# Performance work log

Measured on AMD Instinct MI355X. Metric: run time of the kernel, lower is better.

## Reference

```python
import jax, jax.numpy as jnp
import numpy as np

B = 64           # batch size
N = 512          # number of nodes
E = 1            # edge feature dims of the GSO
M = 256          # nodes carrying edge-variant weights (hybrid EV since M < N)
F = [1, 8, 8]    # node-signal features per layer
K = [3, 3]       # shift taps per layer
MLP = [512, 128] # readout dims
P_EDGE = 0.03    # graph density
ZTOL = 1e-9      # zero tolerance for sparsity pattern


def setup_inputs():
    ks = jax.random.split(jax.random.key(0), 13)
    x = jax.random.normal(ks[0], (B, F[0], N), dtype=jnp.float32)
    adj = (jax.random.uniform(ks[1], (E, N, N)) < P_EDGE).astype(jnp.float32)
    S = adj * jax.random.normal(ks[2], (E, N, N), dtype=jnp.float32) / np.sqrt(N * P_EDGE)

    def w(k, shape, scale):
        return jax.random.normal(k, shape, dtype=jnp.float32) * np.float32(scale)

    wEV1 = w(ks[3], (F[1], E, K[0], F[0], N, N), 1.0 / np.sqrt(F[0] * N))
    wLSI1 = w(ks[4], (F[1], E, K[0], F[0]), 1.0 / np.sqrt(F[0] * K[0]))
    b1 = w(ks[5], (F[1], 1), 0.1)
    wEV2 = w(ks[6], (F[2], E, K[1], F[1], N, N), 1.0 / np.sqrt(F[1] * N))
    wLSI2 = w(ks[7], (F[2], E, K[1], F[1]), 1.0 / np.sqrt(F[1] * K[1]))
    b2 = w(ks[8], (F[2], 1), 0.1)
    W1 = w(ks[9], (MLP[0], F[2] * N), 1.0 / np.sqrt(F[2] * N))
    bW1 = w(ks[10], (MLP[0],), 0.1)
    W2 = w(ks[11], (MLP[1], MLP[0]), 1.0 / np.sqrt(MLP[0]))
    bW2 = w(ks[12], (MLP[1],), 0.1)
    return dict(x=x, S=S, wEV1=wEV1, wLSI1=wLSI1, b1=b1,
                wEV2=wEV2, wLSI2=wLSI2, b2=b2, W1=W1, bW1=bW1, W2=W2, bW2=bW2)


def _sparsity_mask(S):
    # support of S + I, then kill the [M:, M:] block (hybrid EV mask)
    eye = jnp.eye(N, dtype=S.dtype)
    sp = ((jnp.abs(S) + eye[None]) > ZTOL).astype(S.dtype)      # (E,N,N)
    hyb = jnp.ones((N, N), S.dtype).at[M:, M:].set(0.0)
    return sp * hyb[None]


def _ev_layer(xl, S, sp, wEV, wLSI, b):
    # xl: (B,G,N); wEV: (F,E,K,G,N,N); wLSI: (F,E,K,G); b: (F,1)
    Phi = wEV * sp[None, :, None, None]                          # masked filter matrices
    Kl = wEV.shape[2]
    # EV part: y = sum_k Phi^(k) ... Phi^(0) x, summed over e, g
    z = jnp.einsum('fegmn,bgn->bfegm', Phi[:, :, 0], xl)
    y = z
    for k in range(1, Kl):
        z = jnp.einsum('fegmn,bfegn->bfegm', Phi[:, :, k], z)
        y = y + z
    y = y.sum(axis=(2, 3))                                       # (B,F,N)
    # LSI part of the hybrid filter: sum_{e,k,g} h_{fekg} S_e^k x_g
    xe = jnp.broadcast_to(xl[:, None], (xl.shape[0], S.shape[0]) + xl.shape[1:])
    zs = [xe]                                                    # k = 0: identity
    for k in range(1, Kl):
        zs.append(jnp.einsum('emn,begn->begm', S, zs[-1]))
    zst = jnp.stack(zs, axis=2)                                  # (B,E,K,G,N)
    y = y + jnp.einsum('fekg,bekgn->bfn', wLSI, zst)
    return y + b[None]                                           # bias broadcast over nodes


def reference(x, S, wEV1, wLSI1, b1, wEV2, wLSI2, b2, W1, bW1, W2, bW2):
    sp = _sparsity_mask(S)
    # order=None -> permIdentity, so x[:, :, order] == x; NoPool is identity
    y = _ev_layer(x, S, sp, wEV1, wLSI1, b1)
    y = _ev_layer(y, S, sp, wEV2, wLSI2, b2)
    yf = y.reshape(y.shape[0], -1)                               # (B, F[-1]*N)
    h = yf @ W1.T + bW1                                          # linear MLP (no activation)
    return h @ W2.T + bW2
```

## Files before the change

### kernel.cpp

```cpp
#include <hip/hip_runtime.h>
#include <cstdint>
#include <cstddef>

#define NNODE 512
#define MMASK 256
#define ZT 1e-9f

__device__ __forceinline__ float rdl_f(float v, int l) {
  return __uint_as_float(__builtin_amdgcn_readlane(__float_as_uint(v), l));
}

__global__ __launch_bounds__(256) void k_prep(const float* __restrict__ x,
                                              const float* __restrict__ S,
                                              int* __restrict__ sp_col, int* __restrict__ sp_cnt,
                                              int* __restrict__ s_col, float* __restrict__ s_val,
                                              int* __restrict__ s_cnt,
                                              float* __restrict__ xt) {
  int gtid = blockIdx.x * 256 + threadIdx.x;
  int W = gtid >> 6, lane = threadIdx.x & 63;
  {
    int n = gtid >> 6, b = gtid & 63;
    xt[gtid] = x[b * NNODE + n];
  }
  int m = W;
  int csp = 0, cs = 0;
  unsigned long long lt = (1ull << lane) - 1ull;
  for (int ch = 0; ch < 8; ++ch) {
    int n = ch * 64 + lane;
    float s = S[m * NNODE + n];
    bool ps  = (s != 0.f);
    bool psp = ((fabsf(s) + ((m == n) ? 1.f : 0.f)) > ZT) && !((m >= MMASK) && (n >= MMASK));
    unsigned long long msp = __ballot(psp), ms = __ballot(ps);
    if (psp) { int p = csp + __popcll(msp & lt); if (p < 64) sp_col[(m << 6) + p] = n; }
    if (ps)  { int p = cs  + __popcll(ms  & lt); if (p < 64) { s_col[(m << 6) + p] = n; s_val[(m << 6) + p] = s; } }
    csp += __popcll(msp); cs += __popcll(ms);
  }
  if (lane >= csp) sp_col[(m << 6) + lane] = 0;
  if (lane >= cs)  { s_col[(m << 6) + lane] = 0; s_val[(m << 6) + lane] = 0.f; }
  if (lane == 0) { sp_cnt[m] = (csp < 64 ? csp : 64); s_cnt[m] = (cs < 64 ? cs : 64); }
}

__device__ __forceinline__ float ell_mac_rl(int clv, float wgv, int cnt,
                                            const float* __restrict__ zin, int lane) {
  float a0 = 0.f, a1 = 0.f, a2 = 0.f, a3 = 0.f;
  for (int base = 0; base < cnt; base += 16) {
#pragma unroll
    for (int i = 0; i < 16; i += 4) {
      int   c0 = __builtin_amdgcn_readlane(clv, base + i);
      int   c1 = __builtin_amdgcn_readlane(clv, base + i + 1);
      int   c2 = __builtin_amdgcn_readlane(clv, base + i + 2);
      int   c3 = __builtin_amdgcn_readlane(clv, base + i + 3);
      float w0 = rdl_f(wgv, base + i);
      float w1 = rdl_f(wgv, base + i + 1);
      float w2 = rdl_f(wgv, base + i + 2);
      float w3 = rdl_f(wgv, base + i + 3);
      a0 += w0 * zin[(c0 << 6) + lane];
      a1 += w1 * zin[(c1 << 6) + lane];
      a2 += w2 * zin[(c2 << 6) + lane];
      a3 += w3 * zin[(c3 << 6) + lane];
    }
  }
  return (a0 + a1) + (a2 + a3);
}

__device__ __forceinline__ float ell_mac_s(const int* __restrict__ cols,
                                           const float* __restrict__ ws,
                                           int cnt,
                                           const float* __restrict__ zin, int lane) {
  float a0 = 0.f, a1 = 0.f, a2 = 0.f, a3 = 0.f;
  for (int base = 0; base < cnt; base += 16) {
#pragma unroll
    for (int i = 0; i < 16; i += 4) {
      int   c0 = cols[base + i    ]; float w0 = ws[base + i    ];
      int   c1 = cols[base + i + 1]; float w1 = ws[base + i + 1];
      int   c2 = cols[base + i + 2]; float w2 = ws[base + i + 2];
      int   c3 = cols[base + i + 3]; float w3 = ws[base + i + 3];
      a0 += w0 * zin[(c0 << 6) + lane];
      a1 += w1 * zin[(c1 << 6) + lane];
      a2 += w2 * zin[(c2 << 6) + lane];
      a3 += w3 * zin[(c3 << 6) + lane];
    }
  }
  return (a0 + a1) + (a2 + a3);
}

__global__ __launch_bounds__(256) void k_l1s0(const float* __restrict__ wEV1,
    const int* __restrict__ sp_col, const int* __restrict__ sp_cnt,
    const int* __restrict__ s_col, const float* __restrict__ s_val, const int* __restrict__ s_cnt,
    const float* __restrict__ xt, float* __restrict__ zA1, float* __restrict__ u1) {
  int lane = threadIdx.x & 63;
  int W = __builtin_amdgcn_readfirstlane((blockIdx.x * 256 + (int)threadIdx.x) >> 6);
  int nwv = (gridDim.x << 2);
  for (int u = W; u < 4608; u += nwv) {
    if (u < 4096) {
      int f = u >> 9, r = u & 511;
      int clv = sp_col[(r << 6) + lane];
      int cnt = sp_cnt[r];
      const float* wrow = wEV1 + ((size_t)(f * 3 + 0) << 18) + ((size_t)r << 9);
      float wgv = (lane < cnt) ? wrow[clv] : 0.f;
      zA1[((size_t)f << 15) + (r << 6) + lane] = ell_mac_rl(clv, wgv, cnt, xt, lane);
    } else {
      int r = u - 4096;
      u1[(r << 6) + lane] =
          ell_mac_s(s_col + (r << 6), s_val + (r << 6), s_cnt[r], xt, lane);
    }
  }
}

__global__ __launch_bounds__(256) void k_l1s1(const float* __restrict__ wEV1,
    const int* __restrict__ sp_col, const int* __restrict__ sp_cnt,
    const int* __restrict__ s_col, const float* __restrict__ s_val, const int* __restrict__ s_cnt,
    const float* __restrict__ zA1, const float* __restrict__ u1,
    float* __restrict__ zB1, float* __restrict__ u2) {
  int lane = threadIdx.x & 63;
  int W = __builtin_amdgcn_readfirstlane((blockIdx.x * 256 + (int)threadIdx.x) >> 6);
  int nwv = (gridDim.x << 2);
  for (int u = W; u < 4608; u += nwv) {
    if (u < 4096) {
      int f = u >> 9, r = u & 511;
      int clv = sp_col[(r << 6) + lane];
      int cnt = sp_cnt[r];
      const float* wrow = wEV1 + ((size_t)(f * 3 + 1) << 18) + ((size_t)r << 9);
      float wgv = (lane < cnt) ? wrow[clv] : 0.f;
      zB1[((size_t)f << 15) + (r << 6) + lane] =
          ell_mac_rl(clv, wgv, cnt, zA1 + ((size_t)f << 15), lane);
    } else {
      int r = u - 4096;
      u2[(r << 6) + lane] =
          ell_mac_s(s_col + (r << 6), s_val + (r << 6), s_cnt[r], u1, lane);
    }
  }
}

__global__ __launch_bounds__(256) void k_l1s2(const float* __restrict__ wEV1,
    const int* __restrict__ sp_col, const int* __restrict__ sp_cnt,
    const float* __restrict__ zA1, const float* __restrict__ zB1,
    const float* __restrict__ xt, const float* __restrict__ u1, const float* __restrict__ u2,
    const float* __restrict__ wLSI1, const float* __restrict__ b1, float* __restrict__ y1) {
  int lane = threadIdx.x & 63;
  int W = __builtin_amdgcn_readfirstlane((blockIdx.x * 256 + (int)threadIdx.x) >> 6);
  int nwv = (gridDim.x << 2);
  for (int u = W; u < 4096; u += nwv) {
    int f = u >> 9, r = u & 511;
    int clv = sp_col[(r << 6) + lane];
    int cnt = sp_cnt[r];
    const float* wrow = wEV1 + ((size_t)(f * 3 + 2) << 18) + ((size_t)r << 9);
    float wgv = (lane < cnt) ? wrow[clv] : 0.f;
    float a = ell_mac_rl(clv, wgv, cnt, zB1 + ((size_t)f << 15), lane);
    int idx = (r << 6) + lane;
    size_t fi = ((size_t)f << 15) + idx;
    y1[fi] = zA1[fi] + zB1[fi] + a
           + wLSI1[f * 3 + 0] * xt[idx] + wLSI1[f * 3 + 1] * u1[idx]
           + wLSI1[f * 3 + 2] * u2[idx] + b1[f];
  }
}

__global__ __launch_bounds__(256) void k_l2s0(const float* __restrict__ wEV2,
    const int* __restrict__ sp_col, const int* __restrict__ sp_cnt,
    const int* __restrict__ s_col, const float* __restrict__ s_val, const int* __restrict__ s_cnt,
    const float* __restrict__ y1, float* __restrict__ zA2, float* __restrict__ v1) {
  int lane = threadIdx.x & 63;
  int W = __builtin_amdgcn_readfirstlane((blockIdx.x * 256 + (int)threadIdx.x) >> 6);
  int nwv = (gridDim.x << 2);
  for (int u = W; u < 36864; u += nwv) {
    if (u < 32768) {
      int c = u >> 9, r = u & 511;
      int f = c >> 3, g = c & 7;
      int clv = sp_col[(r << 6) + lane];
      int cnt = sp_cnt[r];
      const float* wrow = wEV2 + ((size_t)((f * 3 + 0) * 8 + g) << 18) + ((size_t)r << 9);
      float wgv = (lane < cnt) ? wrow[clv] : 0.f;
      zA2[((size_t)c << 15) + (r << 6) + lane] =
          ell_mac_rl(clv, wgv, cnt, y1 + ((size_t)g << 15), lane);
    } else {
      int t = u - 32768;
      int g = t >> 9, r = t & 511;
      v1[((size_t)g << 15) + (r << 6) + lane] =
          ell_mac_s(s_col + (r << 6), s_val + (r << 6), s_cnt[r],
                    y1 + ((size_t)g << 15), lane);
    }
  }
}

__global__ __launch_bounds__(256) void k_l2s1(const float* __restrict__ wEV2,
    const int* __restrict__ sp_col, const int* __restrict__ sp_cnt,
    const int* __restrict__ s_col, const float* __restrict__ s_val, const int* __restrict__ s_cnt,
    const float* __restrict__ zA2, const float* __restrict__ v1,
    float* __restrict__ zB2, float* __restrict__ v2) {
  int lane = threadIdx.x & 63;
  int W = __builtin_amdgcn_readfirstlane((blockIdx.x * 256 + (int)threadIdx.x) >> 6);
  int nwv = (gridDim.x << 2);
  for (int u = W; u < 36864; u += nwv) {
    if (u < 32768) {
      int c = u >> 9, r = u & 511;
      int f = c >> 3, g = c & 7;
      int clv = sp_col[(r << 6) + lane];
      int cnt = sp_cnt[r];
      const float* wrow = wEV2 + ((size_t)((f * 3 + 1) * 8 + g) << 18) + ((size_t)r << 9);
      float wgv = (lane < cnt) ? wrow[clv] : 0.f;
      zB2[((size_t)c << 15) + (r << 6) + lane] =
          ell_mac_rl(clv, wgv, cnt, zA2 + ((size_t)c << 15), lane);
    } else {
      int t = u - 32768;
      int g = t >> 9, r = t & 511;
      v2[((size_t)g << 15) + (r << 6) + lane] =
          ell_mac_s(s_col + (r << 6), s_val + (r << 6), s_cnt[r],
                    v1 + ((size_t)g << 15), lane);
    }
  }
}

__global__ __launch_bounds__(256) void k_l2s2(const float* __restrict__ wEV2,
    const int* __restrict__ sp_col, const int* __restrict__ sp_cnt,
    const float* __restrict__ zA2, const float* __restrict__ zB2,
    const float* __restrict__ y1, const float* __restrict__ v1, const float* __restrict__ v2,
    const float* __restrict__ wLSI2, const float* __restrict__ b2,
    const float* __restrict__ bW1, float* __restrict__ y2, float* __restrict__ ht) {
  int gtid = blockIdx.x * 256 + threadIdx.x;
  int lane = threadIdx.x & 63;
  int W = __builtin_amdgcn_readfirstlane(gtid >> 6);
  int nwv = (gridDim.x << 2);
  if (gtid < 32768) ht[gtid] = bW1[gtid >> 6];
  for (int u = W; u < 4096; u += nwv) {
    int f = u >> 9, r = u & 511;
    int idx = (r << 6) + lane;
    int clv = sp_col[(r << 6) + lane];
    int cnt = sp_cnt[r];
    float wg[8];
#pragma unroll
    for (int g = 0; g < 8; ++g) {
      const float* wrow = wEV2 + ((size_t)((f * 3 + 2) * 8 + g) << 18) + ((size_t)r << 9);
      wg[g] = (lane < cnt) ? wrow[clv] : 0.f;
    }
    float acc = b2[f];
#pragma unroll
    for (int g = 0; g < 8; ++g) {
      int c = f * 8 + g;
      float a = ell_mac_rl(clv, wg[g], cnt, zB2 + ((size_t)c << 15), lane);
      size_t ci = ((size_t)c << 15) + idx;
      size_t gi = ((size_t)g << 15) + idx;
      acc += zA2[ci] + zB2[ci] + a
           + wLSI2[f * 24 + g]      * y1[gi]
           + wLSI2[f * 24 + 8 + g]  * v1[gi]
           + wLSI2[f * 24 + 16 + g] * v2[gi];
    }
    y2[((size_t)f << 15) + idx] = acc;
  }
}

__global__ __launch_bounds__(256) void k_gemm1(const float* __restrict__ W1,
                                               const float* __restrict__ y2,
                                               const float* __restrict__ bW2,
                                               float* __restrict__ ht,
                                               float* __restrict__ out) {
  int gtid = blockIdx.x * 256 + threadIdx.x;
  int lane = threadIdx.x & 63;
  int W = __builtin_amdgcn_readfirstlane(gtid >> 6);
  int nwv = (gridDim.x << 2);
  if (gtid < 8192) out[gtid] = bW2[gtid & 127];
  for (int u = W; u < 512; u += nwv) {
    int pg = u >> 3, ks = u & 7;
    const float* wrow = W1 + (size_t)pg * 8 * 4096 + ks * 512;
    const float* yb = y2 + ((size_t)(ks * 512) << 6);
    float acc[8] = {0, 0, 0, 0, 0, 0, 0, 0};
    for (int q = 0; q < 512; q += 8) {
      float yv[8];
#pragma unroll
      for (int i = 0; i < 8; ++i) yv[i] = yb[((q + i) << 6) + lane];
#pragma unroll
      for (int i = 0; i < 8; ++i) {
#pragma unroll
        for (int p = 0; p < 8; ++p) acc[p] += wrow[(size_t)p * 4096 + q + i] * yv[i];
      }
    }
#pragma unroll
    for (int p = 0; p < 8; ++p) atomicAdd(&ht[((pg * 8 + p) << 6) + lane], acc[p]);
  }
}

__global__ __launch_bounds__(256) void k_gemm2(const float* __restrict__ W2,
                                               const float* __restrict__ ht,
                                               float* __restrict__ out) {
  int lane = threadIdx.x & 63;
  int W = __builtin_amdgcn_readfirstlane((blockIdx.x * 256 + (int)threadIdx.x) >> 6);
  int nwv = (gridDim.x << 2);
  for (int u = W; u < 1024; u += nwv) {
    int o = u >> 3, qs = u & 7;
    const float* w2 = W2 + (size_t)o * 512 + qs * 64;
    const float* hb = ht + ((size_t)(qs * 64) << 6);
    float acc = 0.f;
    for (int q = 0; q < 64; q += 8) {
#pragma unroll
      for (int i = 0; i < 8; ++i) acc += w2[q + i] * hb[((q + i) << 6) + lane];
    }
    atomicAdd(&out[lane * 128 + o], acc);
  }
}

extern "C" void kernel_launch(void* const* d_in, const int* in_sizes, int n_in,
                              void* d_out, int out_size, void* d_ws, size_t ws_size,
                              hipStream_t stream) {
  const float* x     = (const float*)d_in[0];
  const float* S     = (const float*)d_in[1];
  const float* wEV1  = (const float*)d_in[2];
  const float* wLSI1 = (const float*)d_in[3];
  const float* b1    = (const float*)d_in[4];
  const float* wEV2  = (const float*)d_in[5];
  const float* wLSI2 = (const float*)d_in[6];
  const float* b2    = (const float*)d_in[7];
  const float* W1    = (const float*)d_in[8];
  const float* bW1   = (const float*)d_in[9];
  const float* W2    = (const float*)d_in[10];
  const float* bW2   = (const float*)d_in[11];
  float* out = (float*)d_out;

  char* w = (char*)d_ws;
  auto alloc = [&](size_t bytes) { char* p = w; w += (bytes + 255) & ~(size_t)255; return p; };
  int*   sp_col = (int*)alloc(512 * 64 * 4);
  int*   sp_cnt = (int*)alloc(512 * 4);
  int*   s_col  = (int*)alloc(512 * 64 * 4);
  float* s_val  = (float*)alloc(512 * 64 * 4);
  int*   s_cnt  = (int*)alloc(512 * 4);
  float* xt     = (float*)alloc((size_t)32768 * 4);
  float* u1     = (float*)alloc((size_t)32768 * 4);
  float* u2     = (float*)alloc((size_t)32768 * 4);
  float* zA1    = (float*)alloc((size_t)8 * 32768 * 4);
  float* zB1    = (float*)alloc((size_t)8 * 32768 * 4);
  float* y1     = (float*)alloc((size_t)8 * 32768 * 4);
  float* zA2    = (float*)alloc((size_t)64 * 32768 * 4);
  float* zB2    = (float*)alloc((size_t)64 * 32768 * 4);
  float* v1     = (float*)alloc((size_t)8 * 32768 * 4);
  float* v2     = (float*)alloc((size_t)8 * 32768 * 4);
  float* y2     = (float*)alloc((size_t)8 * 32768 * 4);
  float* ht     = (float*)alloc((size_t)32768 * 4);
  (void)ws_size; (void)in_sizes; (void)n_in; (void)out_size;

  k_prep<<<128, 256, 0, stream>>>(x, S, sp_col, sp_cnt, s_col, s_val, s_cnt, xt);
  k_l1s0<<<1152, 256, 0, stream>>>(wEV1, sp_col, sp_cnt, s_col, s_val, s_cnt, xt, zA1, u1);
  k_l1s1<<<1152, 256, 0, stream>>>(wEV1, sp_col, sp_cnt, s_col, s_val, s_cnt, zA1, u1, zB1, u2);
  k_l1s2<<<1024, 256, 0, stream>>>(wEV1, sp_col, sp_cnt, zA1, zB1, xt, u1, u2, wLSI1, b1, y1);
  k_l2s0<<<9216, 256, 0, stream>>>(wEV2, sp_col, sp_cnt, s_col, s_val, s_cnt, y1, zA2, v1);
  k_l2s1<<<9216, 256, 0, stream>>>(wEV2, sp_col, sp_cnt, s_col, s_val, s_cnt, zA2, v1, zB2, v2);
  k_l2s2<<<1024, 256, 0, stream>>>(wEV2, sp_col, sp_cnt, zA2, zB2, y1, v1, v2, wLSI2, b2, bW1, y2, ht);
  k_gemm1<<<128, 256, 0, stream>>>(W1, y2, bW2, ht, out);
  k_gemm2<<<64, 256, 0, stream>>>(W2, ht, out);
}
```

Before: 396.5 us.

## Prefetch layer-2 edge-variant weights into cache during layer-1 kernels

Layer-1 kernels are enlarged with extra waves that gather the masked wEV2 entries for all three taps, summing them into a dummy register kept alive by an empty asm statement. The goal is to warm the large L2/MALL cache with layer-2 weights while layer-1 runs, so the gathers in the later layer-2 kernels hit cache. The cost is much larger launches and extra memory traffic in layer 1, and the benefit holds only if the prefetched lines survive in cache until layer 2 reads them.

New measurement: 410.2 us. 3.4% more time.

```diff
diff --git a/kernel.cpp b/kernel.cpp
--- a/kernel.cpp
+++ b/kernel.cpp
@@ -84,14 +84,26 @@
   return (a0 + a1) + (a2 + a3);
 }
 
+__device__ __forceinline__ float pf_one(const float* __restrict__ wEV2,
+                                        const int* __restrict__ sp_col,
+                                        const int* __restrict__ sp_cnt,
+                                        int p2, int r, int lane) {
+  int clv = sp_col[(r << 6) + lane];
+  int cnt = sp_cnt[r];
+  const float* wrow = wEV2 + ((size_t)p2 << 18) + ((size_t)r << 9);
+  return (lane < cnt) ? wrow[clv] : 0.f;
+}
+
 __global__ __launch_bounds__(256) void k_l1s0(const float* __restrict__ wEV1,
+    const float* __restrict__ wEV2,
     const int* __restrict__ sp_col, const int* __restrict__ sp_cnt,
     const int* __restrict__ s_col, const float* __restrict__ s_val, const int* __restrict__ s_cnt,
     const float* __restrict__ xt, float* __restrict__ zA1, float* __restrict__ u1) {
   int lane = threadIdx.x & 63;
   int W = __builtin_amdgcn_readfirstlane((blockIdx.x * 256 + (int)threadIdx.x) >> 6);
   int nwv = (gridDim.x << 2);
-  for (int u = W; u < 4608; u += nwv) {
+  float pf = 0.f;
+  for (int u = W; u < 4608 + 32768; u += nwv) {
     if (u < 4096) {
       int f = u >> 9, r = u & 511;
       int clv = sp_col[(r << 6) + lane];
@@ -99,15 +111,20 @@
       const float* wrow = wEV1 + ((size_t)(f * 3 + 0) << 18) + ((size_t)r << 9);
       float wgv = (lane < cnt) ? wrow[clv] : 0.f;
       zA1[((size_t)f << 15) + (r << 6) + lane] = ell_mac_rl(clv, wgv, cnt, xt, lane);
-    } else {
+    } else if (u < 4608) {
       int r = u - 4096;
       u1[(r << 6) + lane] =
           ell_mac_s(s_col + (r << 6), s_val + (r << 6), s_cnt[r], xt, lane);
-    }
-  }
+    } else {
+      int jj = u - 4608;
+      pf += pf_one(wEV2, sp_col, sp_cnt, jj >> 9, jj & 511, lane);
+    }
+  }
+  asm volatile("" :: "v"(pf));
 }
 
 __global__ __launch_bounds__(256) void k_l1s1(const float* __restrict__ wEV1,
+    const float* __restrict__ wEV2,
     const int* __restrict__ sp_col, const int* __restrict__ sp_cnt,
     const int* __restrict__ s_col, const float* __restrict__ s_val, const int* __restrict__ s_cnt,
     const float* __restrict__ zA1, const float* __restrict__ u1,
@@ -115,7 +132,8 @@
   int lane = threadIdx.x & 63;
   int W = __builtin_amdgcn_readfirstlane((blockIdx.x * 256 + (int)threadIdx.x) >> 6);
   int nwv = (gridDim.x << 2);
-  for (int u = W; u < 4608; u += nwv) {
+  float pf = 0.f;
+  for (int u = W; u < 4608 + 32768; u += nwv) {
     if (u < 4096) {
       int f = u >> 9, r = u & 511;
       int clv = sp_col[(r << 6) + lane];
@@ -124,15 +142,20 @@
       float wgv = (lane < cnt) ? wrow[clv] : 0.f;
       zB1[((size_t)f << 15) + (r << 6) + lane] =
           ell_mac_rl(clv, wgv, cnt, zA1 + ((size_t)f << 15), lane);
-    } else {
+    } else if (u < 4608) {
       int r = u - 4096;
       u2[(r << 6) + lane] =
           ell_mac_s(s_col + (r << 6), s_val + (r << 6), s_cnt[r], u1, lane);
-    }
-  }
+    } else {
+      int jj = u - 4608;
+      pf += pf_one(wEV2, sp_col, sp_cnt, 64 + (jj >> 9), jj & 511, lane);
+    }
+  }
+  asm volatile("" :: "v"(pf));
 }
 
 __global__ __launch_bounds__(256) void k_l1s2(const float* __restrict__ wEV1,
+    const float* __restrict__ wEV2,
     const int* __restrict__ sp_col, const int* __restrict__ sp_cnt,
     const float* __restrict__ zA1, const float* __restrict__ zB1,
     const float* __restrict__ xt, const float* __restrict__ u1, const float* __restrict__ u2,
@@ -140,19 +163,26 @@
   int lane = threadIdx.x & 63;
   int W = __builtin_amdgcn_readfirstlane((blockIdx.x * 256 + (int)threadIdx.x) >> 6);
   int nwv = (gridDim.x << 2);
-  for (int u = W; u < 4096; u += nwv) {
-    int f = u >> 9, r = u & 511;
-    int clv = sp_col[(r << 6) + lane];
-    int cnt = sp_cnt[r];
-    const float* wrow = wEV1 + ((size_t)(f * 3 + 2) << 18) + ((size_t)r << 9);
-    float wgv = (lane < cnt) ? wrow[clv] : 0.f;
-    float a = ell_mac_rl(clv, wgv, cnt, zB1 + ((size_t)f << 15), lane);
-    int idx = (r << 6) + lane;
-    size_t fi = ((size_t)f << 15) + idx;
-    y1[fi] = zA1[fi] + zB1[fi] + a
-           + wLSI1[f * 3 + 0] * xt[idx] + wLSI1[f * 3 + 1] * u1[idx]
-           + wLSI1[f * 3 + 2] * u2[idx] + b1[f];
-  }
+  float pf = 0.f;
+  for (int u = W; u < 4096 + 32768; u += nwv) {
+    if (u < 4096) {
+      int f = u >> 9, r = u & 511;
+      int clv = sp_col[(r << 6) + lane];
+      int cnt = sp_cnt[r];
+      const float* wrow = wEV1 + ((size_t)(f * 3 + 2) << 18) + ((size_t)r << 9);
+      float wgv = (lane < cnt) ? wrow[clv] : 0.f;
+      float a = ell_mac_rl(clv, wgv, cnt, zB1 + ((size_t)f << 15), lane);
+      int idx = (r << 6) + lane;
+      size_t fi = ((size_t)f << 15) + idx;
+      y1[fi] = zA1[fi] + zB1[fi] + a
+             + wLSI1[f * 3 + 0] * xt[idx] + wLSI1[f * 3 + 1] * u1[idx]
+             + wLSI1[f * 3 + 2] * u2[idx] + b1[f];
+    } else {
+      int jj = u - 4096;
+      pf += pf_one(wEV2, sp_col, sp_cnt, 128 + (jj >> 9), jj & 511, lane);
+    }
+  }
+  asm volatile("" :: "v"(pf));
 }
 
 __global__ __launch_bounds__(256) void k_l2s0(const float* __restrict__ wEV2,
@@ -336,9 +366,9 @@
   (void)ws_size; (void)in_sizes; (void)n_in; (void)out_size;
 
   k_prep<<<128, 256, 0, stream>>>(x, S, sp_col, sp_cnt, s_col, s_val, s_cnt, xt);
-  k_l1s0<<<1152, 256, 0, stream>>>(wEV1, sp_col, sp_cnt, s_col, s_val, s_cnt, xt, zA1, u1);
-  k_l1s1<<<1152, 256, 0, stream>>>(wEV1, sp_col, sp_cnt, s_col, s_val, s_cnt, zA1, u1, zB1, u2);
-  k_l1s2<<<1024, 256, 0, stream>>>(wEV1, sp_col, sp_cnt, zA1, zB1, xt, u1, u2, wLSI1, b1, y1);
+  k_l1s0<<<9344, 256, 0, stream>>>(wEV1, wEV2, sp_col, sp_cnt, s_col, s_val, s_cnt, xt, zA1, u1);
+  k_l1s1<<<9344, 256, 0, stream>>>(wEV1, wEV2, sp_col, sp_cnt, s_col, s_val, s_cnt, zA1, u1, zB1, u2);
+  k_l1s2<<<9216, 256, 0, stream>>>(wEV1, wEV2, sp_col, sp_cnt, zA1, zB1, xt, u1, u2, wLSI1, b1, y1);
   k_l2s0<<<9216, 256, 0, stream>>>(wEV2, sp_col, sp_cnt, s_col, s_val, s_cnt, y1, zA2, v1);
   k_l2s1<<<9216, 256, 0, stream>>>(wEV2, sp_col, sp_cnt, s_col, s_val, s_cnt, zA2, v1, zB2, v2);
   k_l2s2<<<1024, 256, 0, stream>>>(wEV2, sp_col, sp_cnt, zA2, zB2, y1, v1, v2, wLSI2, b2, bW1, y2, ht);
```
